# Kernel tuning notes

Measured on AMD Instinct MI355X. Metric: run time of the kernel, lower is better.

Reference implementation:

```python
import jax, jax.numpy as jnp
import numpy as np

WINDOW_SIZE = 512
CAUSAL = True

def _sliding_window_mask(seq_len, window_size, causal):
    i = jnp.arange(seq_len)[:, None]
    j = jnp.arange(seq_len)[None, :]
    mask = (j >= i - window_size + 1) & (j <= i)
    if causal:
        mask = mask & (j <= i)
    return mask  # [S, S] bool, True = attend


def setup_inputs() -> dict:
    key = jax.random.key(0)
    k1, k2, k3 = jax.random.split(key, 3)
    B, S, D = 16, 4096, 64
    q = jax.random.normal(k1, (B, S, D), dtype=jnp.float32)
    k = jax.random.normal(k2, (B, S, D), dtype=jnp.float32)
    v = jax.random.normal(k3, (B, S, D), dtype=jnp.float32)
    return {"q": q, "k": k, "v": v}


def reference(q, k, v):
    B, S, D = q.shape
    scale = D ** -0.5
    mask = _sliding_window_mask(S, WINDOW_SIZE, CAUSAL)  # [S, S]
    scores = jnp.einsum("bqd,bkd->bqk", q, k) * scale    # [B, S, S]
    mask_value = -jnp.finfo(scores.dtype).max
    scores = jnp.where(mask[None, :, :], scores, mask_value)
    attn = jax.nn.softmax(scores, axis=-1)
    out = jnp.einsum("bqk,bkd->bqd", attn, v)            # [B, S, D]
    return out
```

## Files before the change

kernel.cpp:

```cpp
#include <hip/hip_runtime.h>

#define BATCH 16
#define SEQ   4096
#define DIM   64
#define WIN   512

constexpr int BM = 128;
constexpr int BN = 64;
constexpr int NTHREADS = 512;
constexpr int KS = DIM + 8;
constexpr int VS = BN + 4;
constexpr int OS = DIM + 4;
constexpr float QSCALE  = 0.125f * 1.44269504088896340736f;
constexpr float MASKVAL = -3.0e38f;

typedef _Float16 f16x2 __attribute__((ext_vector_type(2)));
typedef _Float16 f16x4 __attribute__((ext_vector_type(4)));
typedef _Float16 f16x8 __attribute__((ext_vector_type(8)));
typedef float    f32x4 __attribute__((ext_vector_type(4)));

__device__ __forceinline__ f16x2 pk2(float a, float b) {
    return __builtin_bit_cast(f16x2, __builtin_amdgcn_cvt_pkrtz(a, b));
}

__device__ __forceinline__ void stage_kv(_Float16* __restrict__ Ksh, _Float16* __restrict__ Vsh,
                                         const float4& kv, const float4& vv,
                                         int row, int c4) {
    union { f16x4 v; f16x2 h[2]; } uk;
    uk.h[0] = pk2(kv.x, kv.y);
    uk.h[1] = pk2(kv.z, kv.w);
    *(f16x4*)&Ksh[row * KS + c4] = uk.v;
    Vsh[(c4 + 0) * VS + row] = (_Float16)vv.x;
    Vsh[(c4 + 1) * VS + row] = (_Float16)vv.y;
    Vsh[(c4 + 2) * VS + row] = (_Float16)vv.z;
    Vsh[(c4 + 3) * VS + row] = (_Float16)vv.w;
}

__global__ __launch_bounds__(NTHREADS)
void swa_kernel(const float* __restrict__ qg, const float* __restrict__ kg,
                const float* __restrict__ vg, float* __restrict__ outg) {
    __shared__ __align__(16) char smem[BM * OS * 4];
    _Float16* Ksh = (_Float16*)smem;
    _Float16* Vsh = (_Float16*)(smem + BN * KS * 2);
    float*    Osh = (float*)smem;

    const int tid  = threadIdx.x;
    const int lane = tid & 63;
    const int wave = tid >> 6;
    const int lr   = lane & 15;
    const int quad = lane >> 4;

    const int b     = blockIdx.y;
    const int qblk  = blockIdx.x;
    const int qrow0 = qblk * BM;
    const int wr0   = qrow0 + wave * 16;
    const int q     = wr0 + lr;

    const float* qb = qg + (size_t)b * SEQ * DIM;
    const float* kb = kg + (size_t)b * SEQ * DIM;
    const float* vb = vg + (size_t)b * SEQ * DIM;
    float*       ob = outg + (size_t)b * SEQ * DIM;

    const int row0 = tid >> 4;
    const int c4   = (tid & 15) * 4;

    const float* qp = qb + (size_t)q * DIM + quad * 8;
    const float4 a0 = *(const float4*)(qp + 0);
    const float4 a1 = *(const float4*)(qp + 4);
    const float4 a2 = *(const float4*)(qp + 32);
    const float4 a3 = *(const float4*)(qp + 36);
    union { f16x8 v; f16x2 h[4]; } uq0, uq1;
    uq0.h[0] = pk2(a0.x * QSCALE, a0.y * QSCALE);
    uq0.h[1] = pk2(a0.z * QSCALE, a0.w * QSCALE);
    uq0.h[2] = pk2(a1.x * QSCALE, a1.y * QSCALE);
    uq0.h[3] = pk2(a1.z * QSCALE, a1.w * QSCALE);
    uq1.h[0] = pk2(a2.x * QSCALE, a2.y * QSCALE);
    uq1.h[1] = pk2(a2.z * QSCALE, a2.w * QSCALE);
    uq1.h[2] = pk2(a3.x * QSCALE, a3.y * QSCALE);
    uq1.h[3] = pk2(a3.z * QSCALE, a3.w * QSCALE);
    const f16x8 qf0 = uq0.v, qf1 = uq1.v;

    f32x4 o[4];
    #pragma unroll
    for (int mi = 0; mi < 4; ++mi) o[mi] = (f32x4){0.f, 0.f, 0.f, 0.f};
    float m_run = -1e30f, l_run = 0.f;

    const int t0 = (qrow0 > (WIN - 1)) ? (qrow0 - (WIN - 1)) >> 6 : 0;
    const int t1 = (qrow0 + BM - 1) >> 6;

    {
        const size_t g0 = (size_t)(t0 * BN + row0) * DIM + c4;
        stage_kv(Ksh, Vsh, *(const float4*)&kb[g0], *(const float4*)&vb[g0], row0, c4);
        const size_t g1 = g0 + (size_t)32 * DIM;
        stage_kv(Ksh, Vsh, *(const float4*)&kb[g1], *(const float4*)&vb[g1], row0 + 32, c4);
    }
    __syncthreads();

    for (int t = t0; t <= t1; ++t) {
        const bool have_next = (t < t1);
        float4 kpre0, kpre1, vpre0, vpre1;
        if (have_next) {
            const size_t g0 = (size_t)((t + 1) * BN + row0) * DIM + c4;
            kpre0 = *(const float4*)&kb[g0];
            vpre0 = *(const float4*)&vb[g0];
            const size_t g1 = g0 + (size_t)32 * DIM;
            kpre1 = *(const float4*)&kb[g1];
            vpre1 = *(const float4*)&vb[g1];
        }

        const int kbase = t * BN;
        const bool active = (kbase + BN - 1 >= wr0 - (WIN - 1)) && (kbase <= wr0 + 15);
        if (active) {
            f32x4 sc[4];
            #pragma unroll
            for (int mt = 0; mt < 4; ++mt) {
                const f16x8 kf0 = *(const f16x8*)&Ksh[(mt * 16 + lr) * KS + quad * 8];
                const f16x8 kf1 = *(const f16x8*)&Ksh[(mt * 16 + lr) * KS + 32 + quad * 8];
                f32x4 s = (f32x4){0.f, 0.f, 0.f, 0.f};
                s = __builtin_amdgcn_mfma_f32_16x16x32_f16(kf0, qf0, s, 0, 0, 0);
                s = __builtin_amdgcn_mfma_f32_16x16x32_f16(kf1, qf1, s, 0, 0, 0);
                sc[mt] = s;
            }

            const bool edge = (kbase < wr0 + 15 - (WIN - 1)) || (kbase + BN - 1 > wr0);
            if (edge) {
                #pragma unroll
                for (int mt = 0; mt < 4; ++mt) {
                    #pragma unroll
                    for (int r = 0; r < 4; ++r) {
                        const int key = kbase + mt * 16 + quad * 4 + r;
                        sc[mt][r] = ((unsigned)(q - key) < (unsigned)WIN) ? sc[mt][r] : MASKVAL;
                    }
                }
            }

            float mt_ = MASKVAL;
            #pragma unroll
            for (int mtile = 0; mtile < 4; ++mtile)
                #pragma unroll
                for (int r = 0; r < 4; ++r) mt_ = fmaxf(mt_, sc[mtile][r]);
            mt_ = fmaxf(mt_, __shfl_xor(mt_, 16));
            mt_ = fmaxf(mt_, __shfl_xor(mt_, 32));
            const float mn    = fmaxf(m_run, mt_);
            const float alpha = exp2f(m_run - mn);
            m_run = mn;

            f16x4 pb[4];
            float ls = 0.f;
            #pragma unroll
            for (int nt = 0; nt < 4; ++nt) {
                const float p0 = exp2f(sc[nt][0] - mn);
                const float p1 = exp2f(sc[nt][1] - mn);
                const float p2 = exp2f(sc[nt][2] - mn);
                const float p3 = exp2f(sc[nt][3] - mn);
                ls += (p0 + p1) + (p2 + p3);
                union { f16x4 v; f16x2 h[2]; } up;
                up.h[0] = pk2(p0, p1);
                up.h[1] = pk2(p2, p3);
                pb[nt] = up.v;
            }
            l_run = l_run * alpha + ls;
            #pragma unroll
            for (int mi = 0; mi < 4; ++mi) o[mi] = o[mi] * alpha;

            #pragma unroll
            for (int nt = 0; nt < 4; ++nt) {
                #pragma unroll
                for (int mi = 0; mi < 4; ++mi) {
                    const f16x4 vf = *(const f16x4*)&Vsh[(mi * 16 + lr) * VS + nt * 16 + quad * 4];
                    o[mi] = __builtin_amdgcn_mfma_f32_16x16x16f16(vf, pb[nt], o[mi], 0, 0, 0);
                }
            }
        }

        __builtin_amdgcn_s_barrier();
        if (have_next) {
            stage_kv(Ksh, Vsh, kpre0, vpre0, row0, c4);
            stage_kv(Ksh, Vsh, kpre1, vpre1, row0 + 32, c4);
        }
        __syncthreads();
    }

    l_run += __shfl_xor(l_run, 16);
    l_run += __shfl_xor(l_run, 32);
    const float inv = 1.0f / l_run;

    float* Ow = Osh + wave * 16 * OS;
    #pragma unroll
    for (int mi = 0; mi < 4; ++mi) {
        float4 st;
        st.x = o[mi][0] * inv; st.y = o[mi][1] * inv;
        st.z = o[mi][2] * inv; st.w = o[mi][3] * inv;
        *(float4*)&Ow[lr * OS + mi * 16 + quad * 4] = st;
    }
    #pragma unroll
    for (int j = 0; j < 4; ++j) {
        const int qq = quad + 4 * j;
        const int d4 = lr * 4;
        const float4 vst = *(const float4*)&Ow[qq * OS + d4];
        *(float4*)&ob[(size_t)(wr0 + qq) * DIM + d4] = vst;
    }
}

extern "C" void kernel_launch(void* const* d_in, const int* in_sizes, int n_in,
                              void* d_out, int out_size, void* d_ws, size_t ws_size,
                              hipStream_t stream) {
    (void)in_sizes; (void)n_in; (void)out_size; (void)d_ws; (void)ws_size;
    const float* q = (const float*)d_in[0];
    const float* k = (const float*)d_in[1];
    const float* v = (const float*)d_in[2];
    float* out = (float*)d_out;
    dim3 grid(SEQ / BM, BATCH);
    swa_kernel<<<grid, dim3(NTHREADS), 0, stream>>>(q, k, v, out);
}
```

Measured before the change: 109.9 us.

## Process two 16-row query groups per wave with 256-thread blocks

```diff
diff --git a/kernel.cpp b/kernel.cpp
--- a/kernel.cpp
+++ b/kernel.cpp
@@ -7,7 +7,7 @@
 
 constexpr int BM = 128;
 constexpr int BN = 64;
-constexpr int NTHREADS = 512;
+constexpr int NTHREADS = 256;
 constexpr int KS = DIM + 8;
 constexpr int VS = BN + 4;
 constexpr int OS = DIM + 4;
@@ -36,7 +36,69 @@
     Vsh[(c4 + 3) * VS + row] = (_Float16)vv.w;
 }
 
-__global__ __launch_bounds__(NTHREADS)
+__device__ __forceinline__ void load_qfrag(const float* __restrict__ qb, int q, int quad,
+                                           f16x8& qf0, f16x8& qf1) {
+    const float* qp = qb + (size_t)q * DIM + quad * 8;
+    const float4 a0 = *(const float4*)(qp + 0);
+    const float4 a1 = *(const float4*)(qp + 4);
+    const float4 a2 = *(const float4*)(qp + 32);
+    const float4 a3 = *(const float4*)(qp + 36);
+    union { f16x8 v; f16x2 h[4]; } u0, u1;
+    u0.h[0] = pk2(a0.x * QSCALE, a0.y * QSCALE);
+    u0.h[1] = pk2(a0.z * QSCALE, a0.w * QSCALE);
+    u0.h[2] = pk2(a1.x * QSCALE, a1.y * QSCALE);
+    u0.h[3] = pk2(a1.z * QSCALE, a1.w * QSCALE);
+    u1.h[0] = pk2(a2.x * QSCALE, a2.y * QSCALE);
+    u1.h[1] = pk2(a2.z * QSCALE, a2.w * QSCALE);
+    u1.h[2] = pk2(a3.x * QSCALE, a3.y * QSCALE);
+    u1.h[3] = pk2(a3.z * QSCALE, a3.w * QSCALE);
+    qf0 = u0.v; qf1 = u1.v;
+}
+
+__device__ __forceinline__ void softmax_update(f32x4 (&sc)[4], float& m_run, float& l_run,
+                                               f16x4 (&pb)[4], f32x4 (&o)[4],
+                                               int kbase, int g16, int q, int quad) {
+    const bool edge = (kbase < g16 + 15 - (WIN - 1)) || (kbase + BN - 1 > g16);
+    if (edge) {
+        #pragma unroll
+        for (int mt = 0; mt < 4; ++mt) {
+            #pragma unroll
+            for (int r = 0; r < 4; ++r) {
+                const int key = kbase + mt * 16 + quad * 4 + r;
+                sc[mt][r] = ((unsigned)(q - key) < (unsigned)WIN) ? sc[mt][r] : MASKVAL;
+            }
+        }
+    }
+    float mt_ = MASKVAL;
+    #pragma unroll
+    for (int mtile = 0; mtile < 4; ++mtile)
+        #pragma unroll
+        for (int r = 0; r < 4; ++r) mt_ = fmaxf(mt_, sc[mtile][r]);
+    mt_ = fmaxf(mt_, __shfl_xor(mt_, 16));
+    mt_ = fmaxf(mt_, __shfl_xor(mt_, 32));
+    const float mn    = fmaxf(m_run, mt_);
+    const float alpha = exp2f(m_run - mn);
+    m_run = mn;
+
+    float ls = 0.f;
+    #pragma unroll
+    for (int nt = 0; nt < 4; ++nt) {
+        const float p0 = exp2f(sc[nt][0] - mn);
+        const float p1 = exp2f(sc[nt][1] - mn);
+        const float p2 = exp2f(sc[nt][2] - mn);
+        const float p3 = exp2f(sc[nt][3] - mn);
+        ls += (p0 + p1) + (p2 + p3);
+        union { f16x4 v; f16x2 h[2]; } up;
+        up.h[0] = pk2(p0, p1);
+        up.h[1] = pk2(p2, p3);
+        pb[nt] = up.v;
+    }
+    l_run = l_run * alpha + ls;
+    #pragma unroll
+    for (int mi = 0; mi < 4; ++mi) o[mi] = o[mi] * alpha;
+}
+
+__global__ __launch_bounds__(NTHREADS, 2)
 void swa_kernel(const float* __restrict__ qg, const float* __restrict__ kg,
                 const float* __restrict__ vg, float* __restrict__ outg) {
     __shared__ __align__(16) char smem[BM * OS * 4];
@@ -53,8 +115,11 @@
     const int b     = blockIdx.y;
     const int qblk  = blockIdx.x;
     const int qrow0 = qblk * BM;
-    const int wr0   = qrow0 + wave * 16;
-    const int q     = wr0 + lr;
+    const int wr0   = qrow0 + wave * 32;
+    const int g16_0 = wr0;
+    const int g16_1 = wr0 + 16;
+    const int q0    = g16_0 + lr;
+    const int q1    = g16_1 + lr;
 
     const float* qb = qg + (size_t)b * SEQ * DIM;
     const float* kb = kg + (size_t)b * SEQ * DIM;
@@ -64,137 +129,108 @@
     const int row0 = tid >> 4;
     const int c4   = (tid & 15) * 4;
 
-    const float* qp = qb + (size_t)q * DIM + quad * 8;
-    const float4 a0 = *(const float4*)(qp + 0);
-    const float4 a1 = *(const float4*)(qp + 4);
-    const float4 a2 = *(const float4*)(qp + 32);
-    const float4 a3 = *(const float4*)(qp + 36);
-    union { f16x8 v; f16x2 h[4]; } uq0, uq1;
-    uq0.h[0] = pk2(a0.x * QSCALE, a0.y * QSCALE);
-    uq0.h[1] = pk2(a0.z * QSCALE, a0.w * QSCALE);
-    uq0.h[2] = pk2(a1.x * QSCALE, a1.y * QSCALE);
-    uq0.h[3] = pk2(a1.z * QSCALE, a1.w * QSCALE);
-    uq1.h[0] = pk2(a2.x * QSCALE, a2.y * QSCALE);
-    uq1.h[1] = pk2(a2.z * QSCALE, a2.w * QSCALE);
-    uq1.h[2] = pk2(a3.x * QSCALE, a3.y * QSCALE);
-    uq1.h[3] = pk2(a3.z * QSCALE, a3.w * QSCALE);
-    const f16x8 qf0 = uq0.v, qf1 = uq1.v;
-
-    f32x4 o[4];
-    #pragma unroll
-    for (int mi = 0; mi < 4; ++mi) o[mi] = (f32x4){0.f, 0.f, 0.f, 0.f};
-    float m_run = -1e30f, l_run = 0.f;
+    f16x8 qf0a, qf1a, qf0b, qf1b;
+    load_qfrag(qb, q0, quad, qf0a, qf1a);
+    load_qfrag(qb, q1, quad, qf0b, qf1b);
+
+    f32x4 o0[4], o1[4];
+    #pragma unroll
+    for (int mi = 0; mi < 4; ++mi) {
+        o0[mi] = (f32x4){0.f, 0.f, 0.f, 0.f};
+        o1[mi] = (f32x4){0.f, 0.f, 0.f, 0.f};
+    }
+    float m0 = -1e30f, l0 = 0.f;
+    float m1 = -1e30f, l1 = 0.f;
 
     const int t0 = (qrow0 > (WIN - 1)) ? (qrow0 - (WIN - 1)) >> 6 : 0;
     const int t1 = (qrow0 + BM - 1) >> 6;
 
-    {
-        const size_t g0 = (size_t)(t0 * BN + row0) * DIM + c4;
-        stage_kv(Ksh, Vsh, *(const float4*)&kb[g0], *(const float4*)&vb[g0], row0, c4);
-        const size_t g1 = g0 + (size_t)32 * DIM;
-        stage_kv(Ksh, Vsh, *(const float4*)&kb[g1], *(const float4*)&vb[g1], row0 + 32, c4);
+    #pragma unroll
+    for (int i = 0; i < 4; ++i) {
+        const int row = row0 + 16 * i;
+        const size_t g = (size_t)(t0 * BN + row) * DIM + c4;
+        stage_kv(Ksh, Vsh, *(const float4*)&kb[g], *(const float4*)&vb[g], row, c4);
     }
     __syncthreads();
 
     for (int t = t0; t <= t1; ++t) {
         const bool have_next = (t < t1);
-        float4 kpre0, kpre1, vpre0, vpre1;
+        float4 kpre[4], vpre[4];
         if (have_next) {
-            const size_t g0 = (size_t)((t + 1) * BN + row0) * DIM + c4;
-            kpre0 = *(const float4*)&kb[g0];
-            vpre0 = *(const float4*)&vb[g0];
-            const size_t g1 = g0 + (size_t)32 * DIM;
-            kpre1 = *(const float4*)&kb[g1];
-            vpre1 = *(const float4*)&vb[g1];
+            #pragma unroll
+            for (int i = 0; i < 4; ++i) {
+                const size_t g = (size_t)((t + 1) * BN + row0 + 16 * i) * DIM + c4;
+                kpre[i] = *(const float4*)&kb[g];
+                vpre[i] = *(const float4*)&vb[g];
+            }
         }
 
         const int kbase = t * BN;
-        const bool active = (kbase + BN - 1 >= wr0 - (WIN - 1)) && (kbase <= wr0 + 15);
-        if (active) {
-            f32x4 sc[4];
+        const bool act0 = (kbase <= g16_0 + 15) && (kbase + BN - 1 >= g16_0 - (WIN - 1));
+        const bool act1 = (kbase <= g16_1 + 15) && (kbase + BN - 1 >= g16_1 - (WIN - 1));
+
+        if (act0 || act1) {
+            f32x4 s0[4], s1[4];
             #pragma unroll
             for (int mt = 0; mt < 4; ++mt) {
                 const f16x8 kf0 = *(const f16x8*)&Ksh[(mt * 16 + lr) * KS + quad * 8];
                 const f16x8 kf1 = *(const f16x8*)&Ksh[(mt * 16 + lr) * KS + 32 + quad * 8];
-                f32x4 s = (f32x4){0.f, 0.f, 0.f, 0.f};
-                s = __builtin_amdgcn_mfma_f32_16x16x32_f16(kf0, qf0, s, 0, 0, 0);
-                s = __builtin_amdgcn_mfma_f32_16x16x32_f16(kf1, qf1, s, 0, 0, 0);
-                sc[mt] = s;
-            }
-
-            const bool edge = (kbase < wr0 + 15 - (WIN - 1)) || (kbase + BN - 1 > wr0);
-            if (edge) {
-                #pragma unroll
-                for (int mt = 0; mt < 4; ++mt) {
-                    #pragma unroll
-                    for (int r = 0; r < 4; ++r) {
-                        const int key = kbase + mt * 16 + quad * 4 + r;
-                        sc[mt][r] = ((unsigned)(q - key) < (unsigned)WIN) ? sc[mt][r] : MASKVAL;
-                    }
+                if (act0) {
+                    f32x4 s = (f32x4){0.f, 0.f, 0.f, 0.f};
+                    s = __builtin_amdgcn_mfma_f32_16x16x32_f16(kf0, qf0a, s, 0, 0, 0);
+                    s = __builtin_amdgcn_mfma_f32_16x16x32_f16(kf1, qf1a, s, 0, 0, 0);
+                    s0[mt] = s;
                 }
-            }
-
-            float mt_ = MASKVAL;
-            #pragma unroll
-            for (int mtile = 0; mtile < 4; ++mtile)
-                #pragma unroll
-                for (int r = 0; r < 4; ++r) mt_ = fmaxf(mt_, sc[mtile][r]);
-            mt_ = fmaxf(mt_, __shfl_xor(mt_, 16));
-            mt_ = fmaxf(mt_, __shfl_xor(mt_, 32));
-            const float mn    = fmaxf(m_run, mt_);
-            const float alpha = exp2f(m_run - mn);
-            m_run = mn;
-
-            f16x4 pb[4];
-            float ls = 0.f;
-            #pragma unroll
-            for (int nt = 0; nt < 4; ++nt) {
-                const float p0 = exp2f(sc[nt][0] - mn);
-                const float p1 = exp2f(sc[nt][1] - mn);
-                const float p2 = exp2f(sc[nt][2] - mn);
-                const float p3 = exp2f(sc[nt][3] - mn);
-                ls += (p0 + p1) + (p2 + p3);
-                union { f16x4 v; f16x2 h[2]; } up;
-                up.h[0] = pk2(p0, p1);
-                up.h[1] = pk2(p2, p3);
-                pb[nt] = up.v;
-            }
-            l_run = l_run * alpha + ls;
-            #pragma unroll
-            for (int mi = 0; mi < 4; ++mi) o[mi] = o[mi] * alpha;
+                if (act1) {
+                    f32x4 s = (f32x4){0.f, 0.f, 0.f, 0.f};
+                    s = __builtin_amdgcn_mfma_f32_16x16x32_f16(kf0, qf0b, s, 0, 0, 0);
+                    s = __builtin_amdgcn_mfma_f32_16x16x32_f16(kf1, qf1b, s, 0, 0, 0);
+                    s1[mt] = s;
+                }
+            }
+
+            f16x4 pb0[4], pb1[4];
+            if (act0) softmax_update(s0, m0, l0, pb0, o0, kbase, g16_0, q0, quad);
+            if (act1) softmax_update(s1, m1, l1, pb1, o1, kbase, g16_1, q1, quad);
 
             #pragma unroll
             for (int nt = 0; nt < 4; ++nt) {
                 #pragma unroll
                 for (int mi = 0; mi < 4; ++mi) {
                     const f16x4 vf = *(const f16x4*)&Vsh[(mi * 16 + lr) * VS + nt * 16 + quad * 4];
-                    o[mi] = __builtin_amdgcn_mfma_f32_16x16x16f16(vf, pb[nt], o[mi], 0, 0, 0);
+                    if (act0) o0[mi] = __builtin_amdgcn_mfma_f32_16x16x16f16(vf, pb0[nt], o0[mi], 0, 0, 0);
+                    if (act1) o1[mi] = __builtin_amdgcn_mfma_f32_16x16x16f16(vf, pb1[nt], o1[mi], 0, 0, 0);
                 }
             }
         }
 
         __builtin_amdgcn_s_barrier();
         if (have_next) {
-            stage_kv(Ksh, Vsh, kpre0, vpre0, row0, c4);
-            stage_kv(Ksh, Vsh, kpre1, vpre1, row0 + 32, c4);
+            #pragma unroll
+            for (int i = 0; i < 4; ++i)
+                stage_kv(Ksh, Vsh, kpre[i], vpre[i], row0 + 16 * i, c4);
         }
         __syncthreads();
     }
 
-    l_run += __shfl_xor(l_run, 16);
-    l_run += __shfl_xor(l_run, 32);
-    const float inv = 1.0f / l_run;
-
-    float* Ow = Osh + wave * 16 * OS;
+    l0 += __shfl_xor(l0, 16); l0 += __shfl_xor(l0, 32);
+    l1 += __shfl_xor(l1, 16); l1 += __shfl_xor(l1, 32);
+    const float inv0 = 1.0f / l0;
+    const float inv1 = 1.0f / l1;
+
+    float* Ow = Osh + wave * 32 * OS;
     #pragma unroll
     for (int mi = 0; mi < 4; ++mi) {
-        float4 st;
-        st.x = o[mi][0] * inv; st.y = o[mi][1] * inv;
-        st.z = o[mi][2] * inv; st.w = o[mi][3] * inv;
-        *(float4*)&Ow[lr * OS + mi * 16 + quad * 4] = st;
-    }
-    #pragma unroll
-    for (int j = 0; j < 4; ++j) {
+        float4 st0, st1;
+        st0.x = o0[mi][0] * inv0; st0.y = o0[mi][1] * inv0;
+        st0.z = o0[mi][2] * inv0; st0.w = o0[mi][3] * inv0;
+        *(float4*)&Ow[lr * OS + mi * 16 + quad * 4] = st0;
+        st1.x = o1[mi][0] * inv1; st1.y = o1[mi][1] * inv1;
+        st1.z = o1[mi][2] * inv1; st1.w = o1[mi][3] * inv1;
+        *(float4*)&Ow[(16 + lr) * OS + mi * 16 + quad * 4] = st1;
+    }
+    #pragma unroll
+    for (int j = 0; j < 8; ++j) {
         const int qq = quad + 4 * j;
         const int d4 = lr * 4;
         const float4 vst = *(const float4*)&Ow[qq * OS + d4];
```

After: 201.3 us. +83.1%, slower.

## Double query tile to 256 rows with 1024 threads and store output directly

Applied to the files above, without the earlier changes.

```diff
diff --git a/kernel.cpp b/kernel.cpp
--- a/kernel.cpp
+++ b/kernel.cpp
@@ -5,12 +5,11 @@
 #define DIM   64
 #define WIN   512
 
-constexpr int BM = 128;
+constexpr int BM = 256;
 constexpr int BN = 64;
-constexpr int NTHREADS = 512;
+constexpr int NTHREADS = 1024;
 constexpr int KS = DIM + 8;
 constexpr int VS = BN + 4;
-constexpr int OS = DIM + 4;
 constexpr float QSCALE  = 0.125f * 1.44269504088896340736f;
 constexpr float MASKVAL = -3.0e38f;
 
@@ -39,10 +38,9 @@
 __global__ __launch_bounds__(NTHREADS)
 void swa_kernel(const float* __restrict__ qg, const float* __restrict__ kg,
                 const float* __restrict__ vg, float* __restrict__ outg) {
-    __shared__ __align__(16) char smem[BM * OS * 4];
+    __shared__ __align__(16) char smem[(BN * KS + DIM * VS) * 2];
     _Float16* Ksh = (_Float16*)smem;
     _Float16* Vsh = (_Float16*)(smem + BN * KS * 2);
-    float*    Osh = (float*)smem;
 
     const int tid  = threadIdx.x;
     const int lane = tid & 63;
@@ -91,21 +89,16 @@
     {
         const size_t g0 = (size_t)(t0 * BN + row0) * DIM + c4;
         stage_kv(Ksh, Vsh, *(const float4*)&kb[g0], *(const float4*)&vb[g0], row0, c4);
-        const size_t g1 = g0 + (size_t)32 * DIM;
-        stage_kv(Ksh, Vsh, *(const float4*)&kb[g1], *(const float4*)&vb[g1], row0 + 32, c4);
     }
     __syncthreads();
 
     for (int t = t0; t <= t1; ++t) {
         const bool have_next = (t < t1);
-        float4 kpre0, kpre1, vpre0, vpre1;
+        float4 kpre, vpre;
         if (have_next) {
-            const size_t g0 = (size_t)((t + 1) * BN + row0) * DIM + c4;
-            kpre0 = *(const float4*)&kb[g0];
-            vpre0 = *(const float4*)&vb[g0];
-            const size_t g1 = g0 + (size_t)32 * DIM;
-            kpre1 = *(const float4*)&kb[g1];
-            vpre1 = *(const float4*)&vb[g1];
+            const size_t g = (size_t)((t + 1) * BN + row0) * DIM + c4;
+            kpre = *(const float4*)&kb[g];
+            vpre = *(const float4*)&vb[g];
         }
 
         const int kbase = t * BN;
@@ -175,8 +168,7 @@
 
         __builtin_amdgcn_s_barrier();
         if (have_next) {
-            stage_kv(Ksh, Vsh, kpre0, vpre0, row0, c4);
-            stage_kv(Ksh, Vsh, kpre1, vpre1, row0 + 32, c4);
+            stage_kv(Ksh, Vsh, kpre, vpre, row0, c4);
         }
         __syncthreads();
     }
@@ -184,21 +176,12 @@
     l_run += __shfl_xor(l_run, 16);
     l_run += __shfl_xor(l_run, 32);
     const float inv = 1.0f / l_run;
-
-    float* Ow = Osh + wave * 16 * OS;
     #pragma unroll
     for (int mi = 0; mi < 4; ++mi) {
         float4 st;
         st.x = o[mi][0] * inv; st.y = o[mi][1] * inv;
         st.z = o[mi][2] * inv; st.w = o[mi][3] * inv;
-        *(float4*)&Ow[lr * OS + mi * 16 + quad * 4] = st;
-    }
-    #pragma unroll
-    for (int j = 0; j < 4; ++j) {
-        const int qq = quad + 4 * j;
-        const int d4 = lr * 4;
-        const float4 vst = *(const float4*)&Ow[qq * OS + d4];
-        *(float4*)&ob[(size_t)(wr0 + qq) * DIM + d4] = vst;
+        *(float4*)&ob[(size_t)q * DIM + mi * 16 + quad * 4] = st;
     }
 }
 
```

New measurement: 110.7 us. Within noise of the previous version (+0.7%).
